# Performance work log

Measured on AMD Instinct MI355X. Metric: run time of the kernel, lower is better.

## Reference

```python
import jax, jax.numpy as jnp
import numpy as np

N_NODES = 100000
N_EDGES = 1600000
F_IN = 128
HIDDEN = [128, 128]
F_OUT = 64


def _glorot(key, shape):
    fan_in, fan_out = shape[1], shape[0]
    lim = jnp.sqrt(6.0 / (fan_in + fan_out))
    return jax.random.uniform(key, shape, jnp.float32, -lim, lim)


def setup_inputs() -> dict:
    key = jax.random.key(0)
    ks = jax.random.split(key, 12)
    x = jax.random.normal(ks[0], (N_NODES, F_IN), jnp.float32)
    edge_index = jax.random.randint(ks[1], (2, N_EDGES), 0, N_NODES, jnp.int64)
    dims = [F_IN] + HIDDEN + [F_OUT]  # [128, 128, 128, 64]
    inp = {"x": x, "edge_index": edge_index}
    for i in range(3):
        din, dout = dims[i], dims[i + 1]
        inp[f"Wl{i}"] = _glorot(ks[2 + 3 * i], (dout, din))  # neighbor lin (lin_l)
        inp[f"Wr{i}"] = _glorot(ks[3 + 3 * i], (dout, din))  # root lin (lin_r)
        inp[f"b{i}"] = jnp.zeros((dout,), jnp.float32)
    return inp


def sage_conv(x, src, dst, Wl, Wr, b):
    # PyG SAGEConv, aggr='mean': out = lin_l(mean_{j in N(i)} x_j) + lin_r(x_i) + bias
    msg = x[src]  # [E, Fin] gather from source nodes
    agg = jax.ops.segment_sum(msg, dst, num_segments=N_NODES)  # [N, Fin]
    deg = jax.ops.segment_sum(jnp.ones((src.shape[0],), x.dtype), dst,
                              num_segments=N_NODES)  # [N]
    mean = agg / jnp.maximum(deg, 1.0)[:, None]
    return mean @ Wl.T + x @ Wr.T + b


def reference(x, edge_index, Wl0, Wr0, b0, Wl1, Wr1, b1, Wl2, Wr2, b2):
    src, dst = edge_index[0], edge_index[1]
    h = jax.nn.relu(sage_conv(x, src, dst, Wl0, Wr0, b0))
    h = jax.nn.relu(sage_conv(h, src, dst, Wl1, Wr1, b1))
    out = sage_conv(h, src, dst, Wl2, Wr2, b2)  # final_conv: no relu
    return out
```

## Files before the change

### kernel.cpp

```cpp
#include <hip/hip_runtime.h>

#define NF 128
#define CHUNK 8192

typedef __attribute__((ext_vector_type(8))) short bf16x8;
typedef __attribute__((ext_vector_type(4))) float f32x4;
typedef __attribute__((ext_vector_type(2))) float f32x2;

__device__ __forceinline__ unsigned short f2b(float f) {
    unsigned int u = __float_as_uint(f);
    unsigned int r = (u + 0x7fffu + ((u >> 16) & 1u)) >> 16;
    return (unsigned short)r;
}

__device__ __forceinline__ void gld_lds16(const void* g, const void* l) {
    __builtin_amdgcn_global_load_lds(
        (const __attribute__((address_space(1))) unsigned int*)(unsigned long long)g,
        (__attribute__((address_space(3))) unsigned int*)(unsigned int)(unsigned long long)l,
        16, 0, 0);
}


__global__ __launch_bounds__(256) void prep_kernel(
        const float* __restrict__ x, unsigned short* __restrict__ xb,
        unsigned char* __restrict__ x8, int n4,
        const float* __restrict__ Wl0, const float* __restrict__ Wr0, unsigned short* __restrict__ Wc0,
        const float* __restrict__ Wl1, const float* __restrict__ Wr1, unsigned short* __restrict__ Wc1,
        const float* __restrict__ Wl2, const float* __restrict__ Wr2, const float* __restrict__ b2,
        unsigned short* __restrict__ Wst, float* __restrict__ bst,
        const int* __restrict__ dst, int* __restrict__ hist, int E, int NB,
        int bCvt, int bW0, int bW1, int bWs) {
    __shared__ int hsh[512];
    const int blk = blockIdx.x;
    const int tid = threadIdx.x;
    if (blk < bCvt) {
        int i = blk * 256 + tid;
        if (i < n4) {
            float4 v = *(const float4*)&x[(size_t)i * 4];
            uint2 o;
            o.x = (unsigned int)f2b(v.x) | ((unsigned int)f2b(v.y) << 16);
            o.y = (unsigned int)f2b(v.z) | ((unsigned int)f2b(v.w) << 16);
            *(uint2*)&xb[(size_t)i * 4] = o;
            unsigned p = __builtin_amdgcn_cvt_pk_fp8_f32(v.x, v.y, 0, false);
            p = __builtin_amdgcn_cvt_pk_fp8_f32(v.z, v.w, p, true);
            *(unsigned int*)&x8[(size_t)i * 4] = p;
        }
    } else if (blk < bW1) {
        const bool first = blk < bW0;
        int i = (blk - (first ? bCvt : bW0)) * 256 + tid;
        const float* Wl = first ? Wl0 : Wl1;
        const float* Wr = first ? Wr0 : Wr1;
        unsigned short* Wc = first ? Wc0 : Wc1;
        int f = i >> 7, k = i & 127;
        Wc[f * 256 + k] = f2b(Wl[i]);
        Wc[f * 256 + 128 + k] = f2b(Wr[i]);
    } else if (blk < bWs) {
        int i = (blk - bW1) * 256 + tid;
        int f = i >> 7, k = i & 127;
        Wst[f * 128 + k] = f2b(Wl2[i]);
        Wst[(f + 64) * 128 + k] = f2b(Wr2[i]);
        if (k == 0) {
            bst[f] = 0.f;
            bst[f + 64] = b2[f];
        }
    } else {
        const int hb = blk - bWs;
        for (int i = tid; i < NB; i += 256) hsh[i] = 0;
        __syncthreads();
        const int e0 = hb * CHUNK;
        for (int i = tid; i < CHUNK; i += 256) {
            int e = e0 + i;
            if (e < E) atomicAdd(&hsh[dst[e] >> 8], 1);
        }
        __syncthreads();
        for (int i = tid; i < NB; i += 256) hist[hb * NB + i] = hsh[i];
    }
}


__global__ __launch_bounds__(256) void sb_sum(const int* __restrict__ hist,
                                              int* __restrict__ bsum,
                                              int T, int NB, int NBLK) {
    int i = blockIdx.x * 256 + threadIdx.x;
    int v = 0;
    if (i < T) {
        int b = i / NBLK, blk = i - b * NBLK;
        v = hist[blk * NB + b];
    }
#pragma unroll
    for (int d = 32; d; d >>= 1) v += __shfl_down(v, d, 64);
    __shared__ int wsum[4];
    if ((threadIdx.x & 63) == 0) wsum[threadIdx.x >> 6] = v;
    __syncthreads();
    if (threadIdx.x == 0) bsum[blockIdx.x] = wsum[0] + wsum[1] + wsum[2] + wsum[3];
}

__global__ __launch_bounds__(1024) void sb_scan(const int* __restrict__ bsum,
                                                int* __restrict__ bpre, int NS) {
    __shared__ int s[1024];
    int t = threadIdx.x;
    int v = (t < NS) ? bsum[t] : 0;
    s[t] = v;
    __syncthreads();
    for (int d = 1; d < 1024; d <<= 1) {
        int u = (t >= d) ? s[t - d] : 0;
        __syncthreads();
        s[t] += u;
        __syncthreads();
    }
    if (t < NS) bpre[t] = s[t] - v;
}

__global__ __launch_bounds__(256) void sb_apply(const int* __restrict__ hist,
                                                const int* __restrict__ bpre,
                                                int* __restrict__ base,
                                                int* __restrict__ bstart,
                                                int T, int NB, int NBLK, int E) {
    __shared__ int s[256];
    int i = blockIdx.x * 256 + threadIdx.x;
    int t = threadIdx.x;
    int v = 0;
    int b = 0, blk = 0;
    if (i < T) {
        b = i / NBLK;
        blk = i - b * NBLK;
        v = hist[blk * NB + b];
    }
    s[t] = v;
    __syncthreads();
    for (int d = 1; d < 256; d <<= 1) {
        int u = (t >= d) ? s[t - d] : 0;
        __syncthreads();
        s[t] += u;
        __syncthreads();
    }
    if (i < T) {
        int val = bpre[blockIdx.x] + s[t] - v;
        base[i] = val;
        if (blk == 0) bstart[b] = val;
        if (i == 0) bstart[NB] = E;
    }
}

__global__ __launch_bounds__(256) void scat_kernel(const int* __restrict__ src,
                                                   const int* __restrict__ dst,
                                                   const int* __restrict__ base,
                                                   unsigned int* __restrict__ recs,
                                                   int E, int NB, int NBLK) {
    __shared__ int cur[512];
    const int blk = blockIdx.x;
    for (int b = threadIdx.x; b < NB; b += 256) cur[b] = base[b * NBLK + blk];
    __syncthreads();
    const int e0 = blk * CHUNK;
    for (int i = threadIdx.x; i < CHUNK; i += 256) {
        int e = e0 + i;
        if (e >= E) continue;
        int d = dst[e];
        int b = d >> 8;
        int pos = atomicAdd(&cur[b], 1);
        recs[pos] = (unsigned int)src[e] | ((unsigned int)(d & 255) << 24);
    }
}

__global__ __launch_bounds__(256) void csr_kernel(const unsigned int* __restrict__ recs,
                                                  const int* __restrict__ bstart,
                                                  int* __restrict__ offs,
                                                  float* __restrict__ rdeg,
                                                  int* __restrict__ csr,
                                                  int N, int E) {
    __shared__ int cnt[256];
    __shared__ int sc[256];
    __shared__ int cur[256];
    const int b = blockIdx.x;
    const int t = threadIdx.x;
    const int s0 = bstart[b], s1 = bstart[b + 1];
    cnt[t] = 0;
    __syncthreads();
    for (int i = s0 + t; i < s1; i += 256) atomicAdd(&cnt[recs[i] >> 24], 1);
    __syncthreads();
    int v = cnt[t];
    sc[t] = v;
    __syncthreads();
    for (int d = 1; d < 256; d <<= 1) {
        int u = (t >= d) ? sc[t - d] : 0;
        __syncthreads();
        sc[t] += u;
        __syncthreads();
    }
    int excl = sc[t] - v;
    int node = b * 256 + t;
    if (node < N) {
        offs[node] = s0 + excl;
        rdeg[node] = 1.0f / (float)(v > 1 ? v : 1);
        if (node == N - 1) offs[N] = E;
    }
    cur[t] = s0 + excl;
    __syncthreads();
    for (int i = s0 + t; i < s1; i += 256) {
        unsigned int r = recs[i];
        int pos = atomicAdd(&cur[r >> 24], 1);
        csr[pos] = (int)(r & 0xFFFFFFu);
    }
}


__global__ __launch_bounds__(256) void agg8_kernel(
        const unsigned char* __restrict__ h8, const int* __restrict__ offs,
        const int* __restrict__ csr, const float* __restrict__ rdeg,
        unsigned short* __restrict__ meanout, int N) {
    const int node = blockIdx.x * 4 + (threadIdx.x >> 6);
    const int lane = threadIdx.x & 63;
    if (node >= N) return;
    const int s0 = offs[node], s1 = offs[node + 1];
    const char* __restrict__ hb = (const char*)h8;
    const unsigned lane2 = (unsigned)lane * 2u;
    f32x2 acc = {0.f, 0.f};
    for (int base = s0; base < s1; base += 64) {
        const int cnt = min(64, s1 - base);
        const int boff = csr[base + min(lane, cnt - 1)] << 7;
        int j = 0;
#define AGG8_GROUP(NG)                                                         \
        {                                                                      \
            unsigned o[NG];                                                    \
            _Pragma("unroll")                                                  \
            for (int k = 0; k < NG; ++k)                                       \
                o[k] = (unsigned)__shfl(boff, j + k, 64) + lane2;              \
            unsigned int v[NG];                                                \
            _Pragma("unroll")                                                  \
            for (int k = 0; k < NG; ++k)                                       \
                v[k] = *(const unsigned short*)(hb + o[k]);                    \
            _Pragma("unroll")                                                  \
            for (int k = 0; k < NG; ++k)                                       \
                acc += __builtin_amdgcn_cvt_pk_f32_fp8(v[k], false);           \
            j += NG;                                                           \
        }
        while (j + 16 <= cnt) AGG8_GROUP(16)
        if (cnt & 8) AGG8_GROUP(8)
        if (cnt & 4) AGG8_GROUP(4)
        if (cnt & 2) AGG8_GROUP(2)
        if (cnt & 1) AGG8_GROUP(1)
#undef AGG8_GROUP
    }
    float r = rdeg[node];
    unsigned int o = (unsigned int)f2b(acc.x * r) | ((unsigned int)f2b(acc.y * r) << 16);
    *(unsigned int*)&meanout[(size_t)node * NF + lane * 2] = o;
}


__global__ __launch_bounds__(256) void agg2_kernel(
        const unsigned short* __restrict__ z, const int* __restrict__ offs,
        const int* __restrict__ csr, const float* __restrict__ rdeg,
        float* __restrict__ out, int N) {
    const int node = blockIdx.x * 4 + (threadIdx.x >> 6);
    const int lane = threadIdx.x & 63;
    if (node >= N) return;
    const int s0 = offs[node], s1 = offs[node + 1];
    const char* __restrict__ zb = (const char*)z;
    const unsigned lane2 = (unsigned)lane * 2u;
    float acc = 0.f;
    for (int base = s0; base < s1; base += 64) {
        const int cnt = min(64, s1 - base);
        const int boff = csr[base + min(lane, cnt - 1)] << 8;
        int j = 0;
#define AGG2_GROUP(NG)                                                         \
        {                                                                      \
            unsigned o[NG];                                                    \
            _Pragma("unroll")                                                  \
            for (int k = 0; k < NG; ++k)                                       \
                o[k] = (unsigned)__shfl(boff, j + k, 64) + lane2;              \
            unsigned int v[NG];                                                \
            _Pragma("unroll")                                                  \
            for (int k = 0; k < NG; ++k)                                       \
                v[k] = *(const unsigned short*)(zb + o[k]);                    \
            _Pragma("unroll")                                                  \
            for (int k = 0; k < NG; ++k)                                       \
                acc += __uint_as_float(v[k] << 16);                            \
            j += NG;                                                           \
        }
        while (j + 16 <= cnt) AGG2_GROUP(16)
        if (cnt & 8) AGG2_GROUP(8)
        if (cnt & 4) AGG2_GROUP(4)
        if (cnt & 2) AGG2_GROUP(2)
        if (cnt & 1) AGG2_GROUP(1)
#undef AGG2_GROUP
    }
    float r = rdeg[node];
    unsigned int vr = *(const unsigned short*)(zb + (size_t)node * 256 + 128 + lane2);
    out[(size_t)node * 64 + lane] = acc * r + __uint_as_float(vr << 16);
}


template <bool OUT8>
__global__ __launch_bounds__(256) void gemm_kernel(
        const unsigned short* __restrict__ Abuf,
        const unsigned short* __restrict__ Hbuf,
        const unsigned short* __restrict__ Wcat,
        const float* __restrict__ bias,
        unsigned short* __restrict__ outb,
        unsigned char* __restrict__ out8,
        int N) {
    __shared__ unsigned short As[128 * 256];

    const int tid = threadIdx.x, wid = tid >> 6, lane = tid & 63;
    const int m0 = blockIdx.x * 128;
    char* Ac = (char*)As;
    const char* Ab = (const char*)Abuf;
    const char* Hb = (const char*)Hbuf;
    const char* Wb = (const char*)Wcat;

#pragma unroll
    for (int i = 0; i < 16; ++i) {
        int off = wid * 16384 + i * 1024 + lane * 16;
        int row = off >> 9, c = off & 511;
        int c2 = c ^ ((row & 7) << 4);
        const char* srcp = (c2 < 256) ? (Ab + (size_t)(m0 + row) * 256 + c2)
                                      : (Hb + (size_t)(m0 + row) * 256 + (c2 - 256));
        gld_lds16(srcp, Ac + wid * 16384 + i * 1024);
    }
    asm volatile("s_waitcnt vmcnt(0)" ::: "memory");
    __syncthreads();

    constexpr int MI = 4;
    constexpr int NI = 4;
    const int lm = lane & 15, ko = lane >> 4;
    const int wmBase = (wid >> 1) * 64;
    const int wnBase = (wid & 1) * 64;

    f32x4 acc[MI][NI];
#pragma unroll
    for (int i = 0; i < MI; ++i)
#pragma unroll
        for (int j = 0; j < NI; ++j)
            acc[i][j] = (f32x4){0.f, 0.f, 0.f, 0.f};

#pragma unroll
    for (int ks = 0; ks < 8; ++ks) {
        const int kb = ks * 64 + ko * 16;
        bf16x8 a[MI], b[NI];
#pragma unroll
        for (int j = 0; j < NI; ++j) {
            int row = wnBase + j * 16 + lm;
            b[j] = *(const bf16x8*)(Wb + row * 512 + kb);
        }
#pragma unroll
        for (int i = 0; i < MI; ++i) {
            int row = wmBase + i * 16 + lm;
            a[i] = *(const bf16x8*)(Ac + row * 512 + (kb ^ ((row & 7) << 4)));
        }
#pragma unroll
        for (int i = 0; i < MI; ++i)
#pragma unroll
            for (int j = 0; j < NI; ++j)
                acc[i][j] = __builtin_amdgcn_mfma_f32_16x16x32_bf16(b[j], a[i], acc[i][j], 0, 0, 0);
    }

    __syncthreads();
#pragma unroll
    for (int i = 0; i < MI; ++i) {
        const int r = wmBase + i * 16 + lm;
#pragma unroll
        for (int j = 0; j < NI; ++j) {
            const int col0 = wnBase + j * 16 + ko * 4;
            const float4 bv = *(const float4*)&bias[col0];
            float v0 = fmaxf(acc[i][j][0] + bv.x, 0.f);
            float v1 = fmaxf(acc[i][j][1] + bv.y, 0.f);
            float v2 = fmaxf(acc[i][j][2] + bv.z, 0.f);
            float v3 = fmaxf(acc[i][j][3] + bv.w, 0.f);
            uint2 o;
            o.x = (unsigned int)f2b(v0) | ((unsigned int)f2b(v1) << 16);
            o.y = (unsigned int)f2b(v2) | ((unsigned int)f2b(v3) << 16);
            *(uint2*)(Ac + r * 272 + col0 * 2) = o;
        }
    }
    __syncthreads();
#pragma unroll
    for (int p = 0; p < 8; ++p) {
        const int chunk = tid + p * 256;
        const int row = chunk >> 4;
        const int off = (chunk & 15) * 16;
        const int node = m0 + row;
        if (node >= N) continue;
        uint4 q = *(const uint4*)(Ac + row * 272 + off);
        *(uint4*)((char*)outb + (size_t)node * 256 + off) = q;
        if (OUT8) {
            float f0 = __uint_as_float(q.x << 16), f1 = __uint_as_float(q.x & 0xffff0000u);
            float f2 = __uint_as_float(q.y << 16), f3 = __uint_as_float(q.y & 0xffff0000u);
            float f4 = __uint_as_float(q.z << 16), f5 = __uint_as_float(q.z & 0xffff0000u);
            float f6 = __uint_as_float(q.w << 16), f7 = __uint_as_float(q.w & 0xffff0000u);
            unsigned p0 = __builtin_amdgcn_cvt_pk_fp8_f32(f0, f1, 0, false);
            p0 = __builtin_amdgcn_cvt_pk_fp8_f32(f2, f3, p0, true);
            unsigned p1 = __builtin_amdgcn_cvt_pk_fp8_f32(f4, f5, 0, false);
            p1 = __builtin_amdgcn_cvt_pk_fp8_f32(f6, f7, p1, true);
            uint2 o8 = make_uint2(p0, p1);
            *(uint2*)((char*)out8 + (size_t)node * 128 + (off >> 1)) = o8;
        }
    }
}


__global__ __launch_bounds__(256) void gemmz_kernel(
        const unsigned short* __restrict__ A,
        const unsigned short* __restrict__ W,
        const float* __restrict__ bias,
        unsigned short* __restrict__ outb,
        int N) {
    __shared__ unsigned short As[17408];

    const int tid = threadIdx.x, wid = tid >> 6, lane = tid & 63;
    const int m0 = blockIdx.x * 128;
    char* Ac = (char*)As;
    const char* Ab = (const char*)A;
    const char* Wb = (const char*)W;

#pragma unroll
    for (int i = 0; i < 8; ++i) {
        int off = wid * 8192 + i * 1024 + lane * 16;
        int row = off >> 8, c = off & 255;
        int c2 = c ^ ((row & 7) << 4);
        gld_lds16(Ab + (size_t)(m0 + row) * 256 + c2, Ac + wid * 8192 + i * 1024);
    }
    asm volatile("s_waitcnt vmcnt(0)" ::: "memory");
    __syncthreads();

    const int lm = lane & 15, ko = lane >> 4;
    const int wmBase = (wid >> 1) * 64;
    const int wnBase = (wid & 1) * 64;

    f32x4 acc[4][4];
#pragma unroll
    for (int i = 0; i < 4; ++i)
#pragma unroll
        for (int j = 0; j < 4; ++j)
            acc[i][j] = (f32x4){0.f, 0.f, 0.f, 0.f};

#pragma unroll
    for (int ks = 0; ks < 4; ++ks) {
        const int kb = ks * 64 + ko * 16;
        bf16x8 a[4], b[4];
#pragma unroll
        for (int j = 0; j < 4; ++j) {
            int row = wnBase + j * 16 + lm;
            b[j] = *(const bf16x8*)(Wb + row * 256 + kb);
        }
#pragma unroll
        for (int i = 0; i < 4; ++i) {
            int row = wmBase + i * 16 + lm;
            a[i] = *(const bf16x8*)(Ac + row * 256 + (kb ^ ((row & 7) << 4)));
        }
#pragma unroll
        for (int i = 0; i < 4; ++i)
#pragma unroll
            for (int j = 0; j < 4; ++j)
                acc[i][j] = __builtin_amdgcn_mfma_f32_16x16x32_bf16(b[j], a[i], acc[i][j], 0, 0, 0);
    }

    __syncthreads();
#pragma unroll
    for (int i = 0; i < 4; ++i) {
        const int r = wmBase + i * 16 + lm;
#pragma unroll
        for (int j = 0; j < 4; ++j) {
            const int col0 = wnBase + j * 16 + ko * 4;
            const float4 bv = *(const float4*)&bias[col0];
            uint2 o;
            o.x = (unsigned int)f2b(acc[i][j][0] + bv.x) |
                  ((unsigned int)f2b(acc[i][j][1] + bv.y) << 16);
            o.y = (unsigned int)f2b(acc[i][j][2] + bv.z) |
                  ((unsigned int)f2b(acc[i][j][3] + bv.w) << 16);
            *(uint2*)(Ac + r * 272 + col0 * 2) = o;
        }
    }
    __syncthreads();
#pragma unroll
    for (int p = 0; p < 8; ++p) {
        const int chunk = tid + p * 256;
        const int row = chunk >> 4;
        const int off = (chunk & 15) * 16;
        const int node = m0 + row;
        if (node >= N) continue;
        uint4 q = *(const uint4*)(Ac + row * 272 + off);
        *(uint4*)((char*)outb + (size_t)node * 256 + off) = q;
    }
}


extern "C" void kernel_launch(void* const* d_in, const int* in_sizes, int n_in,
                              void* d_out, int out_size, void* d_ws, size_t ws_size,
                              hipStream_t stream) {
    const float* x   = (const float*)d_in[0];
    const int*   ei  = (const int*)d_in[1];
    const float* Wl0 = (const float*)d_in[2];
    const float* Wr0 = (const float*)d_in[3];
    const float* b0  = (const float*)d_in[4];
    const float* Wl1 = (const float*)d_in[5];
    const float* Wr1 = (const float*)d_in[6];
    const float* b1  = (const float*)d_in[7];
    const float* Wl2 = (const float*)d_in[8];
    const float* Wr2 = (const float*)d_in[9];
    const float* b2  = (const float*)d_in[10];
    float* out = (float*)d_out;

    const int N = in_sizes[0] / NF;
    const int E = in_sizes[1] / 2;
    const int* srcv = ei;
    const int* dstv = ei + E;

    const int NB   = (N + 255) >> 8;
    const int NBLK = (E + CHUNK - 1) / CHUNK;
    const int T    = NB * NBLK;
    const int NS   = (T + 255) / 256;

    char* w = (char*)d_ws;
    auto alloc = [&](size_t bytes) {
        void* p = (void*)w;
        w += (bytes + 255) & ~(size_t)255;
        return p;
    };
    unsigned short* xb   = (unsigned short*)alloc((size_t)N * NF * 2);
    unsigned short* h1b  = (unsigned short*)alloc((size_t)N * NF * 2);
    unsigned short* h2b  = (unsigned short*)alloc((size_t)N * NF * 2);
    unsigned short* mb   = (unsigned short*)alloc((size_t)N * NF * 2);
    unsigned char*  u8   = (unsigned char*)alloc((size_t)N * NF * 2);
    unsigned char*  x8   = u8;
    unsigned char*  h18  = u8 + (size_t)N * NF;
    unsigned short* z2b  = (unsigned short*)u8;
    unsigned short* Wc0  = (unsigned short*)alloc((size_t)128 * 256 * 2);
    unsigned short* Wc1  = (unsigned short*)alloc((size_t)128 * 256 * 2);
    unsigned short* Wst2 = (unsigned short*)alloc((size_t)128 * 128 * 2);
    float*          bst2 = (float*)alloc((size_t)128 * 4);
    int*   offs   = (int*)alloc((size_t)(N + 1) * 4);
    int*   csr    = (int*)alloc((size_t)E * 4);
    float* rdeg   = (float*)alloc((size_t)N * 4);
    unsigned int* recs = (unsigned int*)alloc((size_t)E * 4);
    int*   hist   = (int*)alloc((size_t)T * 4);
    int*   base   = (int*)alloc((size_t)T * 4);
    int*   bstart = (int*)alloc((size_t)(NB + 1) * 4);
    int*   sb1    = (int*)alloc((size_t)1024 * 4);
    int*   sb2    = (int*)alloc((size_t)1024 * 4);

    const int n4 = N * NF / 4;
    const int bCvt = (n4 + 255) / 256;
    const int bW0  = bCvt + 64;
    const int bW1  = bW0 + 64;
    const int bWs  = bW1 + 32;
    const int bTot = bWs + NBLK;

    prep_kernel<<<bTot, 256, 0, stream>>>(x, xb, x8, n4,
                                          Wl0, Wr0, Wc0, Wl1, Wr1, Wc1,
                                          Wl2, Wr2, b2, Wst2, bst2,
                                          dstv, hist, E, NB,
                                          bCvt, bW0, bW1, bWs);
    sb_sum<<<NS, 256, 0, stream>>>(hist, sb1, T, NB, NBLK);
    sb_scan<<<1, 1024, 0, stream>>>(sb1, sb2, NS);
    sb_apply<<<NS, 256, 0, stream>>>(hist, sb2, base, bstart, T, NB, NBLK, E);
    scat_kernel<<<NBLK, 256, 0, stream>>>(srcv, dstv, base, recs, E, NB, NBLK);
    csr_kernel<<<NB, 256, 0, stream>>>(recs, bstart, offs, rdeg, csr, N, E);

    const int ab  = (N + 3) / 4;
    const int gb  = (N + 127) / 128;

    agg8_kernel<<<ab, 256, 0, stream>>>(x8, offs, csr, rdeg, mb, N);
    gemm_kernel<true><<<gb, 256, 0, stream>>>(mb, xb, Wc0, b0, h1b, h18, N);

    agg8_kernel<<<ab, 256, 0, stream>>>(h18, offs, csr, rdeg, mb, N);
    gemm_kernel<false><<<gb, 256, 0, stream>>>(mb, h1b, Wc1, b1, h2b, nullptr, N);

    gemmz_kernel<<<gb, 256, 0, stream>>>(h2b, Wst2, bst2, z2b, N);
    agg2_kernel<<<ab, 256, 0, stream>>>(z2b, offs, csr, rdeg, out, N);
}
```

Before: 278.9 us.

## Retile GEMM kernels to 64x64 output tiles with weights staged in LDS

```diff
diff --git a/kernel.cpp b/kernel.cpp
--- a/kernel.cpp
+++ b/kernel.cpp
@@ -291,7 +291,7 @@
 
 
 template <bool OUT8>
-__global__ __launch_bounds__(256) void gemm_kernel(
+__global__ __launch_bounds__(256, 2) void gemm_kernel(
         const unsigned short* __restrict__ Abuf,
         const unsigned short* __restrict__ Hbuf,
         const unsigned short* __restrict__ Wcat,
@@ -299,69 +299,77 @@
         unsigned short* __restrict__ outb,
         unsigned char* __restrict__ out8,
         int N) {
-    __shared__ unsigned short As[128 * 256];
+    __shared__ char LDS[65536];
 
     const int tid = threadIdx.x, wid = tid >> 6, lane = tid & 63;
-    const int m0 = blockIdx.x * 128;
-    char* Ac = (char*)As;
+    const int half = blockIdx.x & 1;
+    const int m0 = (blockIdx.x >> 1) * 64;
+    const int c0 = half * 64;
+    char* Ac = LDS;
+    char* Wc = LDS + 32768;
     const char* Ab = (const char*)Abuf;
     const char* Hb = (const char*)Hbuf;
     const char* Wb = (const char*)Wcat;
 
 #pragma unroll
-    for (int i = 0; i < 16; ++i) {
-        int off = wid * 16384 + i * 1024 + lane * 16;
+    for (int i = 0; i < 8; ++i) {
+        int off = wid * 8192 + i * 1024 + lane * 16;
         int row = off >> 9, c = off & 511;
         int c2 = c ^ ((row & 7) << 4);
-        const char* srcp = (c2 < 256) ? (Ab + (size_t)(m0 + row) * 256 + c2)
-                                      : (Hb + (size_t)(m0 + row) * 256 + (c2 - 256));
-        gld_lds16(srcp, Ac + wid * 16384 + i * 1024);
+        int g = min(m0 + row, N - 1);
+        const char* srcp = (c2 < 256) ? (Ab + (size_t)g * 256 + c2)
+                                      : (Hb + (size_t)g * 256 + (c2 - 256));
+        gld_lds16(srcp, Ac + wid * 8192 + i * 1024);
+    }
+#pragma unroll
+    for (int i = 0; i < 8; ++i) {
+        int off = wid * 8192 + i * 1024 + lane * 16;
+        int row = off >> 9, c = off & 511;
+        int c2 = c ^ ((row & 7) << 4);
+        gld_lds16(Wb + (size_t)(c0 + row) * 512 + c2, Wc + wid * 8192 + i * 1024);
     }
     asm volatile("s_waitcnt vmcnt(0)" ::: "memory");
     __syncthreads();
 
-    constexpr int MI = 4;
-    constexpr int NI = 4;
     const int lm = lane & 15, ko = lane >> 4;
-    const int wmBase = (wid >> 1) * 64;
-    const int wnBase = (wid & 1) * 64;
-
-    f32x4 acc[MI][NI];
-#pragma unroll
-    for (int i = 0; i < MI; ++i)
-#pragma unroll
-        for (int j = 0; j < NI; ++j)
+    const int wm = wid >> 1, wn = wid & 1;
+
+    f32x4 acc[2][2];
+#pragma unroll
+    for (int i = 0; i < 2; ++i)
+#pragma unroll
+        for (int j = 0; j < 2; ++j)
             acc[i][j] = (f32x4){0.f, 0.f, 0.f, 0.f};
 
 #pragma unroll
     for (int ks = 0; ks < 8; ++ks) {
         const int kb = ks * 64 + ko * 16;
-        bf16x8 a[MI], b[NI];
-#pragma unroll
-        for (int j = 0; j < NI; ++j) {
-            int row = wnBase + j * 16 + lm;
-            b[j] = *(const bf16x8*)(Wb + row * 512 + kb);
-        }
-#pragma unroll
-        for (int i = 0; i < MI; ++i) {
-            int row = wmBase + i * 16 + lm;
+        bf16x8 a[2], b[2];
+#pragma unroll
+        for (int j = 0; j < 2; ++j) {
+            int row = wn * 32 + j * 16 + lm;
+            b[j] = *(const bf16x8*)(Wc + row * 512 + (kb ^ ((row & 7) << 4)));
+        }
+#pragma unroll
+        for (int i = 0; i < 2; ++i) {
+            int row = wm * 32 + i * 16 + lm;
             a[i] = *(const bf16x8*)(Ac + row * 512 + (kb ^ ((row & 7) << 4)));
         }
 #pragma unroll
-        for (int i = 0; i < MI; ++i)
-#pragma unroll
-            for (int j = 0; j < NI; ++j)
+        for (int i = 0; i < 2; ++i)
+#pragma unroll
+            for (int j = 0; j < 2; ++j)
                 acc[i][j] = __builtin_amdgcn_mfma_f32_16x16x32_bf16(b[j], a[i], acc[i][j], 0, 0, 0);
     }
 
     __syncthreads();
 #pragma unroll
-    for (int i = 0; i < MI; ++i) {
-        const int r = wmBase + i * 16 + lm;
-#pragma unroll
-        for (int j = 0; j < NI; ++j) {
-            const int col0 = wnBase + j * 16 + ko * 4;
-            const float4 bv = *(const float4*)&bias[col0];
+    for (int i = 0; i < 2; ++i) {
+        const int r = wm * 32 + i * 16 + lm;
+#pragma unroll
+        for (int j = 0; j < 2; ++j) {
+            const int lcol = wn * 32 + j * 16 + ko * 4;
+            const float4 bv = *(const float4*)&bias[c0 + lcol];
             float v0 = fmaxf(acc[i][j][0] + bv.x, 0.f);
             float v1 = fmaxf(acc[i][j][1] + bv.y, 0.f);
             float v2 = fmaxf(acc[i][j][2] + bv.z, 0.f);
@@ -369,19 +377,19 @@
             uint2 o;
             o.x = (unsigned int)f2b(v0) | ((unsigned int)f2b(v1) << 16);
             o.y = (unsigned int)f2b(v2) | ((unsigned int)f2b(v3) << 16);
-            *(uint2*)(Ac + r * 272 + col0 * 2) = o;
-        }
-    }
-    __syncthreads();
-#pragma unroll
-    for (int p = 0; p < 8; ++p) {
+            *(uint2*)(Ac + r * 144 + lcol * 2) = o;
+        }
+    }
+    __syncthreads();
+#pragma unroll
+    for (int p = 0; p < 2; ++p) {
         const int chunk = tid + p * 256;
-        const int row = chunk >> 4;
-        const int off = (chunk & 15) * 16;
+        const int row = chunk >> 3;
+        const int off = (chunk & 7) * 16;
         const int node = m0 + row;
         if (node >= N) continue;
-        uint4 q = *(const uint4*)(Ac + row * 272 + off);
-        *(uint4*)((char*)outb + (size_t)node * 256 + off) = q;
+        uint4 q = *(const uint4*)(Ac + row * 144 + off);
+        *(uint4*)((char*)outb + (size_t)node * 256 + c0 * 2 + off) = q;
         if (OUT8) {
             float f0 = __uint_as_float(q.x << 16), f1 = __uint_as_float(q.x & 0xffff0000u);
             float f2 = __uint_as_float(q.y << 16), f3 = __uint_as_float(q.y & 0xffff0000u);
@@ -392,94 +400,104 @@
             unsigned p1 = __builtin_amdgcn_cvt_pk_fp8_f32(f4, f5, 0, false);
             p1 = __builtin_amdgcn_cvt_pk_fp8_f32(f6, f7, p1, true);
             uint2 o8 = make_uint2(p0, p1);
-            *(uint2*)((char*)out8 + (size_t)node * 128 + (off >> 1)) = o8;
-        }
-    }
-}
-
-
-__global__ __launch_bounds__(256) void gemmz_kernel(
+            *(uint2*)((char*)out8 + (size_t)node * 128 + c0 + (off >> 1)) = o8;
+        }
+    }
+}
+
+
+__global__ __launch_bounds__(256, 2) void gemmz_kernel(
         const unsigned short* __restrict__ A,
         const unsigned short* __restrict__ W,
         const float* __restrict__ bias,
         unsigned short* __restrict__ outb,
         int N) {
-    __shared__ unsigned short As[17408];
+    __shared__ char LDS[32768];
 
     const int tid = threadIdx.x, wid = tid >> 6, lane = tid & 63;
-    const int m0 = blockIdx.x * 128;
-    char* Ac = (char*)As;
+    const int half = blockIdx.x & 1;
+    const int m0 = (blockIdx.x >> 1) * 64;
+    const int c0 = half * 64;
+    char* Ac = LDS;
+    char* Wc = LDS + 16384;
     const char* Ab = (const char*)A;
     const char* Wb = (const char*)W;
 
 #pragma unroll
-    for (int i = 0; i < 8; ++i) {
-        int off = wid * 8192 + i * 1024 + lane * 16;
+    for (int i = 0; i < 4; ++i) {
+        int off = wid * 4096 + i * 1024 + lane * 16;
         int row = off >> 8, c = off & 255;
         int c2 = c ^ ((row & 7) << 4);
-        gld_lds16(Ab + (size_t)(m0 + row) * 256 + c2, Ac + wid * 8192 + i * 1024);
+        int g = min(m0 + row, N - 1);
+        gld_lds16(Ab + (size_t)g * 256 + c2, Ac + wid * 4096 + i * 1024);
+    }
+#pragma unroll
+    for (int i = 0; i < 4; ++i) {
+        int off = wid * 4096 + i * 1024 + lane * 16;
+        int row = off >> 8, c = off & 255;
+        int c2 = c ^ ((row & 7) << 4);
+        gld_lds16(Wb + (size_t)(c0 + row) * 256 + c2, Wc + wid * 4096 + i * 1024);
     }
     asm volatile("s_waitcnt vmcnt(0)" ::: "memory");
     __syncthreads();
 
     const int lm = lane & 15, ko = lane >> 4;
-    const int wmBase = (wid >> 1) * 64;
-    const int wnBase = (wid & 1) * 64;
-
-    f32x4 acc[4][4];
-#pragma unroll
-    for (int i = 0; i < 4; ++i)
-#pragma unroll
-        for (int j = 0; j < 4; ++j)
+    const int wm = wid >> 1, wn = wid & 1;
+
+    f32x4 acc[2][2];
+#pragma unroll
+    for (int i = 0; i < 2; ++i)
+#pragma unroll
+        for (int j = 0; j < 2; ++j)
             acc[i][j] = (f32x4){0.f, 0.f, 0.f, 0.f};
 
 #pragma unroll
     for (int ks = 0; ks < 4; ++ks) {
         const int kb = ks * 64 + ko * 16;
-        bf16x8 a[4], b[4];
-#pragma unroll
-        for (int j = 0; j < 4; ++j) {
-            int row = wnBase + j * 16 + lm;
-            b[j] = *(const bf16x8*)(Wb + row * 256 + kb);
-        }
-#pragma unroll
-        for (int i = 0; i < 4; ++i) {
-            int row = wmBase + i * 16 + lm;
+        bf16x8 a[2], b[2];
+#pragma unroll
+        for (int j = 0; j < 2; ++j) {
+            int row = wn * 32 + j * 16 + lm;
+            b[j] = *(const bf16x8*)(Wc + row * 256 + (kb ^ ((row & 7) << 4)));
+        }
+#pragma unroll
+        for (int i = 0; i < 2; ++i) {
+            int row = wm * 32 + i * 16 + lm;
             a[i] = *(const bf16x8*)(Ac + row * 256 + (kb ^ ((row & 7) << 4)));
         }
 #pragma unroll
-        for (int i = 0; i < 4; ++i)
-#pragma unroll
-            for (int j = 0; j < 4; ++j)
+        for (int i = 0; i < 2; ++i)
+#pragma unroll
+            for (int j = 0; j < 2; ++j)
                 acc[i][j] = __builtin_amdgcn_mfma_f32_16x16x32_bf16(b[j], a[i], acc[i][j], 0, 0, 0);
     }
 
     __syncthreads();
 #pragma unroll
-    for (int i = 0; i < 4; ++i) {
-        const int r = wmBase + i * 16 + lm;
-#pragma unroll
-        for (int j = 0; j < 4; ++j) {
-            const int col0 = wnBase + j * 16 + ko * 4;
-            const float4 bv = *(const float4*)&bias[col0];
+    for (int i = 0; i < 2; ++i) {
+        const int r = wm * 32 + i * 16 + lm;
+#pragma unroll
+        for (int j = 0; j < 2; ++j) {
+            const int lcol = wn * 32 + j * 16 + ko * 4;
+            const float4 bv = *(const float4*)&bias[c0 + lcol];
             uint2 o;
             o.x = (unsigned int)f2b(acc[i][j][0] + bv.x) |
                   ((unsigned int)f2b(acc[i][j][1] + bv.y) << 16);
             o.y = (unsigned int)f2b(acc[i][j][2] + bv.z) |
                   ((unsigned int)f2b(acc[i][j][3] + bv.w) << 16);
-            *(uint2*)(Ac + r * 272 + col0 * 2) = o;
-        }
-    }
-    __syncthreads();
-#pragma unroll
-    for (int p = 0; p < 8; ++p) {
+            *(uint2*)(Ac + r * 144 + lcol * 2) = o;
+        }
+    }
+    __syncthreads();
+#pragma unroll
+    for (int p = 0; p < 2; ++p) {
         const int chunk = tid + p * 256;
-        const int row = chunk >> 4;
-        const int off = (chunk & 15) * 16;
+        const int row = chunk >> 3;
+        const int off = (chunk & 7) * 16;
         const int node = m0 + row;
         if (node >= N) continue;
-        uint4 q = *(const uint4*)(Ac + row * 272 + off);
-        *(uint4*)((char*)outb + (size_t)node * 256 + off) = q;
+        uint4 q = *(const uint4*)(Ac + row * 144 + off);
+        *(uint4*)((char*)outb + (size_t)node * 256 + c0 * 2 + off) = q;
     }
 }
 
@@ -557,14 +575,14 @@
     csr_kernel<<<NB, 256, 0, stream>>>(recs, bstart, offs, rdeg, csr, N, E);
 
     const int ab  = (N + 3) / 4;
-    const int gb  = (N + 127) / 128;
+    const int gb2 = 2 * ((N + 63) / 64);
 
     agg8_kernel<<<ab, 256, 0, stream>>>(x8, offs, csr, rdeg, mb, N);
-    gemm_kernel<true><<<gb, 256, 0, stream>>>(mb, xb, Wc0, b0, h1b, h18, N);
+    gemm_kernel<true><<<gb2, 256, 0, stream>>>(mb, xb, Wc0, b0, h1b, h18, N);
 
     agg8_kernel<<<ab, 256, 0, stream>>>(h18, offs, csr, rdeg, mb, N);
-    gemm_kernel<false><<<gb, 256, 0, stream>>>(mb, h1b, Wc1, b1, h2b, nullptr, N);
-
-    gemmz_kernel<<<gb, 256, 0, stream>>>(h2b, Wst2, bst2, z2b, N);
+    gemm_kernel<false><<<gb2, 256, 0, stream>>>(mb, h1b, Wc1, b1, h2b, nullptr, N);
+
+    gemmz_kernel<<<gb2, 256, 0, stream>>>(h2b, Wst2, bst2, z2b, N);
     agg2_kernel<<<ab, 256, 0, stream>>>(z2b, offs, csr, rdeg, out, N);
 }
```

Measured after the change: 258.8 us. 1.08x faster.
